# Kernel tuning notes

Measured on AMD Instinct MI355X. Metric: run time of the kernel, lower is better.

Reference implementation:

```python
import jax, jax.numpy as jnp
import numpy as np

N_HEADS = 16
SEG = 64
EPS = 1e-6


def _sigma(x):
    # ELU(x) + 1 kernel feature map (strictly positive)
    return jax.nn.elu(x) + 1.0


def setup_inputs() -> dict:
    key = jax.random.key(0)
    kx, kq, kk, kv, ko = jax.random.split(key, 5)
    B, T, D = 4, 4096, 1024
    scale = D ** -0.5
    return {
        "x": jax.random.normal(kx, (B, T, D), dtype=jnp.float32),
        "W_q": jax.random.normal(kq, (D, D), dtype=jnp.float32) * scale,
        "W_k": jax.random.normal(kk, (D, D), dtype=jnp.float32) * scale,
        "W_v": jax.random.normal(kv, (D, D), dtype=jnp.float32) * scale,
        "W_o": jax.random.normal(ko, (D, D), dtype=jnp.float32) * scale,
        "beta_param": jnp.zeros((N_HEADS,), dtype=jnp.float32),
    }


def _infini_attention(x, W_q, W_k, W_v, W_o, beta_param):
    B, T, D = x.shape
    H = N_HEADS
    dk = D // H
    assert T % SEG == 0
    S = T // SEG

    def proj(W):
        # nn.Linear: x @ W.T ; split heads -> (B,H,T,dk) -> (S,B,H,SEG,dk)
        y = (x @ W.T).reshape(B, T, H, dk).transpose(0, 2, 1, 3)
        return y.reshape(B, H, S, SEG, dk).transpose(2, 0, 1, 3, 4)

    Qs, Ks, Vs = proj(W_q), proj(W_k), proj(W_v)

    beta = jax.nn.sigmoid(beta_param).reshape(1, H, 1, 1)
    causal = jnp.triu(jnp.ones((SEG, SEG), dtype=bool), k=1)
    inv_sqrt_dk = 1.0 / jnp.sqrt(jnp.asarray(dk, x.dtype))

    M0 = jnp.zeros((B, H, dk, dk), dtype=x.dtype)
    z0 = jnp.zeros((B, H, dk), dtype=x.dtype)

    def step(carry, qkv):
        M, z = carry
        q, k, v = qkv  # each (B,H,SEG,dk)
        # Eq.4 memory retrieval
        sq = _sigma(q)
        denom_q = jnp.sum(sq * z[:, :, None, :], axis=-1, keepdims=True) + EPS
        A_mem = jnp.matmul(sq, M) / denom_q
        # local causal softmax attention
        scores = jnp.matmul(q, jnp.swapaxes(k, -2, -1)) * inv_sqrt_dk
        scores = jnp.where(causal, -jnp.inf, scores)
        A_dot = jnp.matmul(jax.nn.softmax(scores, axis=-1), v)
        A_s = beta * A_mem + (1.0 - beta) * A_dot
        # Eq.5 delta-rule memory update
        sk = _sigma(k)
        denom_k = jnp.sum(sk * z[:, :, None, :], axis=-1, keepdims=True) + EPS
        V_prev = jnp.matmul(sk, M) / denom_k
        M_new = M + jnp.einsum("bhtk,bhtv->bhkv", sk, v - V_prev)
        z_new = z + jnp.sum(sk, axis=-2)
        return (M_new, z_new), A_s

    (M, z), outs = jax.lax.scan(step, (M0, z0), (Qs, Ks, Vs))
    # outs: (S,B,H,SEG,dk) -> (B,T,D)
    out = outs.transpose(1, 3, 0, 2, 4).reshape(B, S * SEG, H, dk)
    # careful: need segment-major time ordering -> (B, H, T, dk) then (B,T,H,dk)
    out = outs.transpose(1, 2, 0, 3, 4).reshape(B, H, T, dk)
    out = out.transpose(0, 2, 1, 3).reshape(B, T, D)
    out = out @ W_o.T
    return out, M.mean(0), z.mean(0)


def reference(x, W_q, W_k, W_v, W_o, beta_param):
    return _infini_attention(x, W_q, W_k, W_v, W_o, beta_param)
```

## Files before the change

### kernel.cpp

```cpp
#include <hip/hip_runtime.h>

typedef __bf16 bf16_t;
typedef __bf16 bf16x8 __attribute__((ext_vector_type(8)));
typedef __bf16 bf16x4 __attribute__((ext_vector_type(4)));
typedef float  f32x4  __attribute__((ext_vector_type(4)));

__device__ __forceinline__ void gload16(const bf16_t* g, bf16_t* l) {
    __builtin_amdgcn_global_load_lds(
        (const __attribute__((address_space(1))) void*)(g),
        (__attribute__((address_space(3))) void*)(l), 16, 0, 0);
}

__global__ __launch_bounds__(256) void cast_bf16_kernel(const float* __restrict__ in,
                                                        bf16_t* __restrict__ out, int n4) {
    int i = blockIdx.x * 256 + threadIdx.x;
    if (i >= n4) return;
    f32x4 v = *reinterpret_cast<const f32x4*>(in + (size_t)i * 4);
    bf16x4 o;
    o[0] = (bf16_t)v[0]; o[1] = (bf16_t)v[1]; o[2] = (bf16_t)v[2]; o[3] = (bf16_t)v[3];
    *reinterpret_cast<bf16x4*>(out + (size_t)i * 4) = o;
}

__global__ __launch_bounds__(256) void cast4_kernel(const float* __restrict__ w0,
                                                    const float* __restrict__ w1,
                                                    const float* __restrict__ w2,
                                                    const float* __restrict__ w3,
                                                    bf16_t* __restrict__ o0,
                                                    bf16_t* __restrict__ o1,
                                                    bf16_t* __restrict__ o2,
                                                    bf16_t* __restrict__ o3) {
    int which = blockIdx.x >> 10;
    int i = (blockIdx.x & 1023) * 256 + threadIdx.x;
    const float* in = (which == 0) ? w0 : (which == 1) ? w1 : (which == 2) ? w2 : w3;
    bf16_t*     out = (which == 0) ? o0 : (which == 1) ? o1 : (which == 2) ? o2 : o3;
    f32x4 v = *reinterpret_cast<const f32x4*>(in + (size_t)i * 4);
    bf16x4 o;
    o[0] = (bf16_t)v[0]; o[1] = (bf16_t)v[1]; o[2] = (bf16_t)v[2]; o[3] = (bf16_t)v[3];
    *reinterpret_cast<bf16x4*>(out + (size_t)i * 4) = o;
}

__device__ __forceinline__ bf16x8 sigma8(bf16x8 x) {
    bf16x8 o;
#pragma unroll
    for (int j = 0; j < 8; j++) {
        float f = (float)x[j];
        float sg = f > 0.f ? f + 1.f : __expf(f);
        o[j] = (bf16_t)sg;
    }
    return o;
}

template <int OUT_BF16>
__global__ __launch_bounds__(512, 2) void gemm256(const bf16_t* __restrict__ A,
                                                  const bf16_t* __restrict__ Bm,
                                                  void* __restrict__ Cv,
                                                  int M, int N, int K) {
    __shared__ bf16_t As[4][256 * 32];
    __shared__ bf16_t Bs[4][256 * 32];

    int bid = blockIdx.x;
    int xq = bid & 7, jq = bid >> 3;
    int bm = xq * 8 + (jq >> 2), bn = jq & 3;

    int tid = threadIdx.x;
    int w = tid >> 6, lane = tid & 63;
    int wm = w >> 2, wn = w & 3;
    int lr = lane & 15, lk = lane >> 4;

    int srow = lane >> 2;
    int schunk = (lane & 3) ^ ((lane >> 3) & 3);
    const bf16_t* gA0 = A  + (size_t)(bm * 256 + w * 32 + srow) * K + schunk * 8;
    const bf16_t* gA1 = gA0 + (size_t)16 * K;
    const bf16_t* gB0 = Bm + (size_t)(bn * 256 + w * 32 + srow) * K + schunk * 8;
    const bf16_t* gB1 = gB0 + (size_t)16 * K;
    int lO0 = (w * 32) * 32 + lane * 8;
    int lO1 = (w * 32 + 16) * 32 + lane * 8;

    int chunkb = (lk ^ ((lr >> 1) & 3)) << 4;
    int aoff[8], boff[4];
#pragma unroll
    for (int mi = 0; mi < 8; mi++) aoff[mi] = (wm * 128 + mi * 16 + lr) * 64 + chunkb;
#pragma unroll
    for (int ni = 0; ni < 4; ni++) boff[ni] = (wn * 64 + ni * 16 + lr) * 64 + chunkb;

    f32x4 acc[8][4];
#pragma unroll
    for (int mi = 0; mi < 8; mi++)
#pragma unroll
        for (int ni = 0; ni < 4; ni++) acc[mi][ni] = (f32x4){0.f, 0.f, 0.f, 0.f};

    const int NT = K >> 5;

    auto STAGE = [&](int t) {
        int slot = t & 3;
        size_t ko = (size_t)t * 32;
        gload16(gA0 + ko, &As[slot][lO0]);
        gload16(gA1 + ko, &As[slot][lO1]);
        gload16(gB0 + ko, &Bs[slot][lO0]);
        gload16(gB1 + ko, &Bs[slot][lO1]);
    };

    STAGE(0); STAGE(1); STAGE(2);

#pragma unroll 1
    for (int t = 0; t < NT; ++t) {
        int ahead = NT - 1 - t;
        if (ahead >= 2)      asm volatile("s_waitcnt vmcnt(8)" ::: "memory");
        else if (ahead == 1) asm volatile("s_waitcnt vmcnt(4)" ::: "memory");
        else                 asm volatile("s_waitcnt vmcnt(0)" ::: "memory");
        __builtin_amdgcn_sched_barrier(0);
        __builtin_amdgcn_s_barrier();
        __builtin_amdgcn_sched_barrier(0);

        const char* pa = (const char*)(&As[t & 3][0]);
        const char* pb = (const char*)(&Bs[t & 3][0]);
        bf16x8 af[8], bfr[4];
#pragma unroll
        for (int mi = 0; mi < 8; mi++)
            af[mi] = *reinterpret_cast<const bf16x8*>(pa + aoff[mi]);
#pragma unroll
        for (int ni = 0; ni < 4; ni++)
            bfr[ni] = *reinterpret_cast<const bf16x8*>(pb + boff[ni]);

        if (t + 3 < NT) STAGE(t + 3);

        asm volatile("s_waitcnt lgkmcnt(0)" ::: "memory");
        __builtin_amdgcn_sched_barrier(0);
        __builtin_amdgcn_s_setprio(1);
#pragma unroll
        for (int mi = 0; mi < 8; mi++)
#pragma unroll
            for (int ni = 0; ni < 4; ni++)
                acc[mi][ni] = __builtin_amdgcn_mfma_f32_16x16x32_bf16(af[mi], bfr[ni], acc[mi][ni], 0, 0, 0);
        __builtin_amdgcn_s_setprio(0);
    }

    int row0 = bm * 256 + wm * 128 + lk * 4;
    int col0 = bn * 256 + wn * 64 + lr;
#pragma unroll
    for (int mi = 0; mi < 8; mi++)
#pragma unroll
        for (int ni = 0; ni < 4; ni++)
#pragma unroll
            for (int jj = 0; jj < 4; jj++) {
                size_t idx = (size_t)(row0 + mi * 16 + jj) * N + (col0 + ni * 16);
                float v = acc[mi][ni][jj];
                if (OUT_BF16) reinterpret_cast<bf16_t*>(Cv)[idx] = (bf16_t)v;
                else          reinterpret_cast<float*>(Cv)[idx]  = v;
            }
}

__global__ __launch_bounds__(256) void attn_kernel(const bf16_t* __restrict__ Qb,
                                                   bf16_t* __restrict__ Kb,
                                                   bf16_t* __restrict__ Vb,
                                                   bf16_t* __restrict__ skTg,
                                                   float* __restrict__ csum,
                                                   bf16_t* __restrict__ Adot) {
    __shared__ bf16_t kS[64 * 72];
    __shared__ bf16_t vS[64 * 72];
    __shared__ bf16_t skT[64 * 72];
    __shared__ bf16_t vT[64 * 72];
    __shared__ bf16_t pS[64 * 72];
    __shared__ float  scr[64 * 68];

    int u = blockIdx.x;
    int bh = u >> 6, s = u & 63;
    int b = bh >> 4, h = bh & 15;
    int tid = threadIdx.x;
    int w = tid >> 6, lane = tid & 63;
    int lr = lane & 15, lk = lane >> 4;
    int r = tid >> 2, qd = tid & 3, c0 = qd << 4;

    size_t vseg = ((size_t)b * 4096 + s * 64) * 1024 + (size_t)h * 64;
    size_t sb = ((size_t)bh * 64 + s) * 4096;

    {
        bf16x8 k0 = *reinterpret_cast<const bf16x8*>(Kb + vseg + (size_t)r * 1024 + c0);
        bf16x8 k1 = *reinterpret_cast<const bf16x8*>(Kb + vseg + (size_t)r * 1024 + c0 + 8);
        bf16x8 v0 = *reinterpret_cast<const bf16x8*>(Vb + vseg + (size_t)r * 1024 + c0);
        bf16x8 v1 = *reinterpret_cast<const bf16x8*>(Vb + vseg + (size_t)r * 1024 + c0 + 8);
        *reinterpret_cast<bf16x8*>(&kS[r * 72 + c0])     = k0;
        *reinterpret_cast<bf16x8*>(&kS[r * 72 + c0 + 8]) = k1;
        *reinterpret_cast<bf16x8*>(&vS[r * 72 + c0])     = v0;
        *reinterpret_cast<bf16x8*>(&vS[r * 72 + c0 + 8]) = v1;
        bf16x8 s0 = sigma8(k0), s1 = sigma8(k1);
        *reinterpret_cast<bf16x8*>(Kb + vseg + (size_t)r * 1024 + c0)     = s0;
        *reinterpret_cast<bf16x8*>(Kb + vseg + (size_t)r * 1024 + c0 + 8) = s1;
#pragma unroll
        for (int j = 0; j < 8; j++) {
            skT[(c0 + j) * 72 + r]     = s0[j];
            skT[(c0 + 8 + j) * 72 + r] = s1[j];
            vT[(c0 + j) * 72 + r]      = v0[j];
            vT[(c0 + 8 + j) * 72 + r]  = v1[j];
        }
    }
    __syncthreads();

    if (tid < 64) {
        float acc = 0.f;
#pragma unroll 8
        for (int t = 0; t < 64; t++) acc += (float)skT[tid * 72 + t];
        csum[((size_t)bh * 64 + s) * 64 + tid] = acc;
    }
    *reinterpret_cast<bf16x8*>(skTg + sb + (size_t)r * 64 + c0) =
        *reinterpret_cast<const bf16x8*>(&skT[r * 72 + c0]);
    *reinterpret_cast<bf16x8*>(skTg + sb + (size_t)r * 64 + c0 + 8) =
        *reinterpret_cast<const bf16x8*>(&skT[r * 72 + c0 + 8]);
    *reinterpret_cast<bf16x8*>(Vb + vseg + (size_t)r * 1024 + c0) =
        *reinterpret_cast<const bf16x8*>(&vT[r * 72 + c0]);
    *reinterpret_cast<bf16x8*>(Vb + vseg + (size_t)r * 1024 + c0 + 8) =
        *reinterpret_cast<const bf16x8*>(&vT[r * 72 + c0 + 8]);

    {
        bf16x8 aq[2];
#pragma unroll
        for (int ks = 0; ks < 2; ks++)
            aq[ks] = *reinterpret_cast<const bf16x8*>(Qb + vseg + (size_t)(w * 16 + lr) * 1024 + lk * 8 + ks * 32);
        f32x4 sc[4];
#pragma unroll
        for (int ct = 0; ct < 4; ct++) {
            sc[ct] = (f32x4){0.f, 0.f, 0.f, 0.f};
#pragma unroll
            for (int ks = 0; ks < 2; ks++) {
                bf16x8 bfrag = *reinterpret_cast<const bf16x8*>(&kS[(ct * 16 + lr) * 72 + lk * 8 + ks * 32]);
                sc[ct] = __builtin_amdgcn_mfma_f32_16x16x32_bf16(aq[ks], bfrag, sc[ct], 0, 0, 0);
            }
        }
#pragma unroll
        for (int ct = 0; ct < 4; ct++)
#pragma unroll
            for (int j = 0; j < 4; j++)
                scr[(w * 16 + lk * 4 + j) * 68 + ct * 16 + lr] = sc[ct][j] * 0.125f;
    }
    __syncthreads();

    {
        float p[16];
        float mx = -3.4e38f;
        const float* srow_p = &scr[r * 68 + c0];
#pragma unroll
        for (int i = 0; i < 16; i++) {
            int c = c0 + i;
            float v = (c <= r) ? srow_p[i] : -3.4e38f;
            p[i] = v;
            mx = fmaxf(mx, v);
        }
        mx = fmaxf(mx, __shfl_xor(mx, 1));
        mx = fmaxf(mx, __shfl_xor(mx, 2));
        float sum = 0.f;
#pragma unroll
        for (int i = 0; i < 16; i++) {
            int c = c0 + i;
            float e = (c <= r) ? __expf(p[i] - mx) : 0.f;
            p[i] = e;
            sum += e;
        }
        sum += __shfl_xor(sum, 1);
        sum += __shfl_xor(sum, 2);
        float inv = 1.f / sum;
        bf16x8 p0, p1;
#pragma unroll
        for (int j = 0; j < 8; j++) {
            p0[j] = (bf16_t)(p[j] * inv);
            p1[j] = (bf16_t)(p[8 + j] * inv);
        }
        *reinterpret_cast<bf16x8*>(&pS[r * 72 + c0])     = p0;
        *reinterpret_cast<bf16x8*>(&pS[r * 72 + c0 + 8]) = p1;
    }
    __syncthreads();

    {
        f32x4 ad[4];
#pragma unroll
        for (int ct = 0; ct < 4; ct++) {
            ad[ct] = (f32x4){0.f, 0.f, 0.f, 0.f};
#pragma unroll
            for (int ks = 0; ks < 2; ks++) {
                bf16x8 afrag = *reinterpret_cast<const bf16x8*>(&pS[(w * 16 + lr) * 72 + lk * 8 + ks * 32]);
                bf16x8 bfrag = *reinterpret_cast<const bf16x8*>(&vT[(ct * 16 + lr) * 72 + lk * 8 + ks * 32]);
                ad[ct] = __builtin_amdgcn_mfma_f32_16x16x32_bf16(afrag, bfrag, ad[ct], 0, 0, 0);
            }
        }
#pragma unroll
        for (int ct = 0; ct < 4; ct++)
#pragma unroll
            for (int j = 0; j < 4; j++)
                kS[(w * 16 + lk * 4 + j) * 72 + ct * 16 + lr] = (bf16_t)ad[ct][j];
    }
    __syncthreads();
    *reinterpret_cast<bf16x8*>(Adot + sb + (size_t)r * 64 + c0) =
        *reinterpret_cast<const bf16x8*>(&kS[r * 72 + c0]);
    *reinterpret_cast<bf16x8*>(Adot + sb + (size_t)r * 64 + c0 + 8) =
        *reinterpret_cast<const bf16x8*>(&kS[r * 72 + c0 + 8]);
}

__global__ __launch_bounds__(64) void zprefix_kernel(const float* __restrict__ csum,
                                                     float* __restrict__ zx,
                                                     float* __restrict__ zfin) {
    int bh = blockIdx.x;
    int d = threadIdx.x;
    float c[64];
#pragma unroll
    for (int s = 0; s < 64; s++)
        c[s] = csum[((size_t)bh * 64 + s) * 64 + d];
    float z = 0.f;
#pragma unroll
    for (int s = 0; s < 64; s++) {
        zx[((size_t)bh * 64 + s) * 64 + d] = z;
        z += c[s];
    }
    zfin[bh * 64 + d] = z;
}

__global__ __launch_bounds__(128) void denom_kernel(const bf16_t* __restrict__ Qb,
                                                    const bf16_t* __restrict__ sK,
                                                    const float* __restrict__ zx,
                                                    float* __restrict__ invq,
                                                    float* __restrict__ invk) {
    __shared__ float zL[64];
    int u = blockIdx.x;
    int bh = u >> 6, s = u & 63;
    int b = bh >> 4, h = bh & 15;
    int tid = threadIdx.x;
    if (tid < 64) zL[tid] = zx[((size_t)bh * 64 + s) * 64 + tid];
    __syncthreads();
    int row = tid & 63;
    bool isq = tid < 64;
    const bf16_t* src = (isq ? Qb : sK) +
                        ((size_t)b * 4096 + s * 64 + row) * 1024 + (size_t)h * 64;
    float acc = 0.f;
#pragma unroll
    for (int blk = 0; blk < 8; blk++) {
        bf16x8 v = *reinterpret_cast<const bf16x8*>(src + blk * 8);
#pragma unroll
        for (int j = 0; j < 8; j++) {
            float f = (float)v[j];
            float sg;
            if (isq) {
                sg = f > 0.f ? f + 1.f : __expf(f);
                sg = (float)(bf16_t)sg;
            } else {
                sg = f;
            }
            acc = __builtin_fmaf(sg, zL[blk * 8 + j], acc);
        }
    }
    float inv = 1.f / (acc + 1e-6f);
    float* dst = isq ? invq : invk;
    dst[((size_t)bh * 64 + s) * 64 + row] = inv;
}

__global__ __launch_bounds__(64, 1) void scan_kernel(const bf16_t* __restrict__ sK,
                                                     const bf16_t* __restrict__ vTg,
                                                     const bf16_t* __restrict__ skTg,
                                                     const float* __restrict__ invk,
                                                     bf16_t* __restrict__ Msnap,
                                                     float* __restrict__ Mfin) {
    __shared__ bf16_t MbL[16 * 72];
    __shared__ bf16_t uTL[16 * 72];
    __shared__ float  ikL[64];

    int blk = blockIdx.x;
    int bh = blk & 63, cq = blk >> 6;
    int c0 = cq << 4;
    int b = bh >> 4, h = bh & 15;
    int lane = threadIdx.x;
    int lr = lane & 15, lk = lane >> 4;
    int vr = lane >> 2, vt0 = (lane & 3) << 4;

    size_t chbase = ((size_t)b * 4096) * 1024 + (size_t)h * 64;
    size_t stbase = (size_t)bh * 64 * 4096;

    auto swz = [](bf16_t* base, int row, int intra) -> bf16_t* {
        return (bf16_t*)((char*)base + row * 144 + (intra ^ ((row & 7) << 4)));
    };

    for (int i = lane; i < 16 * 72; i += 64) MbL[i] = (bf16_t)0.f;
    f32x4 Mreg[4];
#pragma unroll
    for (int rt = 0; rt < 4; rt++) Mreg[rt] = (f32x4){0.f, 0.f, 0.f, 0.f};

    bf16x8 cK[4][2], cT[4][2];
#pragma unroll
    for (int rt = 0; rt < 4; rt++)
#pragma unroll
        for (int ks = 0; ks < 2; ks++) {
            cK[rt][ks] = *reinterpret_cast<const bf16x8*>(
                sK + chbase + (size_t)(rt * 16 + lr) * 1024 + lk * 8 + ks * 32);
            cT[rt][ks] = *reinterpret_cast<const bf16x8*>(
                skTg + stbase + (size_t)(rt * 16 + lr) * 64 + lk * 8 + ks * 32);
        }
    {
        bf16x8 v0 = *reinterpret_cast<const bf16x8*>(vTg + chbase + (size_t)(c0 + vr) * 1024 + vt0);
        bf16x8 v1 = *reinterpret_cast<const bf16x8*>(vTg + chbase + (size_t)(c0 + vr) * 1024 + vt0 + 8);
        *reinterpret_cast<bf16x8*>(swz(uTL, vr, vt0 * 2))      = v0;
        *reinterpret_cast<bf16x8*>(swz(uTL, vr, vt0 * 2 + 16)) = v1;
        ikL[lane] = invk[(size_t)bh * 4096 + lane];
    }

    for (int s = 0; s < 64; s++) {
        bf16x8 nK[4][2], nT[4][2], nv0, nv1;
        float nik = 0.f;
        if (s < 63) {
            size_t vs2 = chbase + (size_t)(s + 1) * 65536;
            size_t sb2 = stbase + (size_t)(s + 1) * 4096;
#pragma unroll
            for (int rt = 0; rt < 4; rt++)
#pragma unroll
                for (int ks = 0; ks < 2; ks++) {
                    nK[rt][ks] = *reinterpret_cast<const bf16x8*>(
                        sK + vs2 + (size_t)(rt * 16 + lr) * 1024 + lk * 8 + ks * 32);
                    nT[rt][ks] = *reinterpret_cast<const bf16x8*>(
                        skTg + sb2 + (size_t)(rt * 16 + lr) * 64 + lk * 8 + ks * 32);
                }
            nv0 = *reinterpret_cast<const bf16x8*>(vTg + vs2 + (size_t)(c0 + vr) * 1024 + vt0);
            nv1 = *reinterpret_cast<const bf16x8*>(vTg + vs2 + (size_t)(c0 + vr) * 1024 + vt0 + 8);
            nik = invk[(size_t)bh * 4096 + (size_t)(s + 1) * 64 + lane];
        }

        bf16x8 mb0 = *reinterpret_cast<const bf16x8*>(swz(MbL, lr, lk * 16));
        bf16x8 mb1 = *reinterpret_cast<const bf16x8*>(swz(MbL, lr, lk * 16 + 64));
        f32x4 Y[4];
#pragma unroll
        for (int rt = 0; rt < 4; rt++) {
            Y[rt] = (f32x4){0.f, 0.f, 0.f, 0.f};
            Y[rt] = __builtin_amdgcn_mfma_f32_16x16x32_bf16(cK[rt][0], mb0, Y[rt], 0, 0, 0);
            Y[rt] = __builtin_amdgcn_mfma_f32_16x16x32_bf16(cK[rt][1], mb1, Y[rt], 0, 0, 0);
        }

#pragma unroll
        for (int rt = 0; rt < 4; rt++) {
            bf16x4 vv = *reinterpret_cast<const bf16x4*>(swz(uTL, lr, rt * 32 + lk * 8));
            bf16x4 uu;
#pragma unroll
            for (int j = 0; j < 4; j++) {
                float ik = ikL[rt * 16 + lk * 4 + j];
                uu[j] = (bf16_t)((float)vv[j] - Y[rt][j] * ik);
            }
            *reinterpret_cast<bf16x4*>(swz(uTL, lr, rt * 32 + lk * 8)) = uu;
        }

        bf16x8 ub0 = *reinterpret_cast<const bf16x8*>(swz(uTL, lr, lk * 16));
        bf16x8 ub1 = *reinterpret_cast<const bf16x8*>(swz(uTL, lr, lk * 16 + 64));
#pragma unroll
        for (int rt = 0; rt < 4; rt++) {
            Mreg[rt] = __builtin_amdgcn_mfma_f32_16x16x32_bf16(cT[rt][0], ub0, Mreg[rt], 0, 0, 0);
            Mreg[rt] = __builtin_amdgcn_mfma_f32_16x16x32_bf16(cT[rt][1], ub1, Mreg[rt], 0, 0, 0);
        }

#pragma unroll
        for (int rt = 0; rt < 4; rt++) {
            bf16x4 mp;
#pragma unroll
            for (int j = 0; j < 4; j++) mp[j] = (bf16_t)Mreg[rt][j];
            *reinterpret_cast<bf16x4*>(swz(MbL, lr, rt * 32 + lk * 8)) = mp;
            if (s < 63)
                *reinterpret_cast<bf16x4*>(
                    Msnap + (((size_t)bh * 64 + s + 1) * 64 + c0 + lr) * 64 + rt * 16 + lk * 4) = mp;
        }

        if (s < 63) {
#pragma unroll
            for (int rt = 0; rt < 4; rt++)
#pragma unroll
                for (int ks = 0; ks < 2; ks++) { cK[rt][ks] = nK[rt][ks]; cT[rt][ks] = nT[rt][ks]; }
            *reinterpret_cast<bf16x8*>(swz(uTL, vr, vt0 * 2))      = nv0;
            *reinterpret_cast<bf16x8*>(swz(uTL, vr, vt0 * 2 + 16)) = nv1;
            ikL[lane] = nik;
        }
    }

#pragma unroll
    for (int rt = 0; rt < 4; rt++)
#pragma unroll
        for (int j = 0; j < 4; j++)
            Mfin[(size_t)bh * 4096 + (size_t)(rt * 16 + lk * 4 + j) * 64 + c0 + lr] = Mreg[rt][j];
}

__global__ __launch_bounds__(256) void combine_kernel(const bf16_t* __restrict__ Qb,
                                                      const bf16_t* __restrict__ Msnap,
                                                      const bf16_t* __restrict__ Adot,
                                                      const float* __restrict__ invq,
                                                      const float* __restrict__ beta_param,
                                                      bf16_t* __restrict__ Op) {
    __shared__ bf16_t oS[64 * 72];
    __shared__ bf16_t adS[64 * 72];
    __shared__ float  iq[64];

    int u = blockIdx.x;
    int bh = u >> 6, s = u & 63;
    int b = bh >> 4, h = bh & 15;
    int tid = threadIdx.x;
    int w = tid >> 6, lane = tid & 63;
    int lr = lane & 15, lk = lane >> 4;
    int r = tid >> 2, c0 = (tid & 3) << 4;

    size_t vseg = ((size_t)b * 4096 + s * 64) * 1024 + (size_t)h * 64;
    size_t sb = ((size_t)bh * 64 + s) * 4096;
    size_t ib = ((size_t)bh * 64 + s) * 64;

    float beta = 1.f / (1.f + __expf(-beta_param[h]));
    float omb = 1.f - beta;

    *reinterpret_cast<bf16x8*>(&adS[r * 72 + c0]) =
        *reinterpret_cast<const bf16x8*>(Adot + sb + (size_t)r * 64 + c0);
    *reinterpret_cast<bf16x8*>(&adS[r * 72 + c0 + 8]) =
        *reinterpret_cast<const bf16x8*>(Adot + sb + (size_t)r * 64 + c0 + 8);
    if (tid < 64) iq[tid] = invq[ib + tid];

    f32x4 Y[4];
#pragma unroll
    for (int ct = 0; ct < 4; ct++) Y[ct] = (f32x4){0.f, 0.f, 0.f, 0.f};
    if (s > 0) {
        bf16x8 aq[2];
#pragma unroll
        for (int ks = 0; ks < 2; ks++)
            aq[ks] = sigma8(*reinterpret_cast<const bf16x8*>(
                Qb + vseg + (size_t)(w * 16 + lr) * 1024 + lk * 8 + ks * 32));
#pragma unroll
        for (int ct = 0; ct < 4; ct++)
#pragma unroll
            for (int ks = 0; ks < 2; ks++) {
                bf16x8 bfrag = *reinterpret_cast<const bf16x8*>(
                    Msnap + sb + (size_t)(ct * 16 + lr) * 64 + lk * 8 + ks * 32);
                Y[ct] = __builtin_amdgcn_mfma_f32_16x16x32_bf16(aq[ks], bfrag, Y[ct], 0, 0, 0);
            }
    }
    __syncthreads();

#pragma unroll
    for (int ct = 0; ct < 4; ct++) {
        int colc = ct * 16 + lr;
#pragma unroll
        for (int j = 0; j < 4; j++) {
            int t = w * 16 + lk * 4 + j;
            float o = beta * (Y[ct][j] * iq[t]) + omb * (float)adS[t * 72 + colc];
            oS[t * 72 + colc] = (bf16_t)o;
        }
    }
    __syncthreads();

    *reinterpret_cast<bf16x8*>(Op + vseg + (size_t)r * 1024 + c0) =
        *reinterpret_cast<const bf16x8*>(&oS[r * 72 + c0]);
    *reinterpret_cast<bf16x8*>(Op + vseg + (size_t)r * 1024 + c0 + 8) =
        *reinterpret_cast<const bf16x8*>(&oS[r * 72 + c0 + 8]);
}

__global__ __launch_bounds__(256) void mean_kernel(const float* __restrict__ Mfin,
                                                   const float* __restrict__ zfin,
                                                   float* __restrict__ out) {
    int idx = blockIdx.x * 256 + threadIdx.x;
    if (idx < 65536) {
        out[16777216 + idx] = 0.25f * (Mfin[idx] + Mfin[idx + 65536] +
                                       Mfin[idx + 131072] + Mfin[idx + 196608]);
    } else if (idx < 66560) {
        int j = idx - 65536;
        out[16842752 + j] = 0.25f * (zfin[j] + zfin[j + 1024] + zfin[j + 2048] + zfin[j + 3072]);
    }
}

extern "C" void kernel_launch(void* const* d_in, const int* in_sizes, int n_in,
                              void* d_out, int out_size, void* d_ws, size_t ws_size,
                              hipStream_t stream) {
    const float* x      = (const float*)d_in[0];
    const float* Wq     = (const float*)d_in[1];
    const float* Wk     = (const float*)d_in[2];
    const float* Wv     = (const float*)d_in[3];
    const float* Wo     = (const float*)d_in[4];
    const float* beta_p = (const float*)d_in[5];
    float* out = (float*)d_out;
    char* ws = (char*)d_ws;

    const size_t NX = 16777216ull;

    bf16_t* xb   = (bf16_t*)ws;
    bf16_t* Adot = xb;
    bf16_t* Wqb  = (bf16_t*)(ws + 33554432);
    bf16_t* Wkb  = (bf16_t*)(ws + 35651584);
    bf16_t* Wvb  = (bf16_t*)(ws + 37748736);
    bf16_t* Wob  = (bf16_t*)(ws + 39845888);
    bf16_t* Qb   = (bf16_t*)(ws + 41943040);
    bf16_t* Kb   = (bf16_t*)(ws + 75497472);
    bf16_t* Vb   = (bf16_t*)(ws + 109051904);
    bf16_t* skT  = (bf16_t*)(ws + 142606336);
    bf16_t* Op   = (bf16_t*)(ws + 176160768);
    float*  csum = (float*)(ws + 209715200);
    float*  zx   = (float*)(ws + 210763776);
    float*  invq = (float*)(ws + 211812352);
    float*  invk = (float*)(ws + 212860928);
    float*  Mfin = (float*)(ws + 213909504);
    float*  zfin = (float*)(ws + 214958080);
    bf16_t* Msnap = (bf16_t*)d_out;

    cast_bf16_kernel<<<dim3(16384), dim3(256), 0, stream>>>(x, xb, (int)(NX / 4));
    cast4_kernel<<<dim3(4096), dim3(256), 0, stream>>>(Wq, Wk, Wv, Wo, Wqb, Wkb, Wvb, Wob);

    gemm256<1><<<dim3(256), dim3(512), 0, stream>>>(xb, Wqb, (void*)Qb, 16384, 1024, 1024);
    gemm256<1><<<dim3(256), dim3(512), 0, stream>>>(xb, Wkb, (void*)Kb, 16384, 1024, 1024);
    gemm256<1><<<dim3(256), dim3(512), 0, stream>>>(xb, Wvb, (void*)Vb, 16384, 1024, 1024);

    attn_kernel<<<dim3(4096), dim3(256), 0, stream>>>(Qb, Kb, Vb, skT, csum, Adot);
    zprefix_kernel<<<dim3(64), dim3(64), 0, stream>>>(csum, zx, zfin);
    denom_kernel<<<dim3(4096), dim3(128), 0, stream>>>(Qb, Kb, zx, invq, invk);
    scan_kernel<<<dim3(256), dim3(64), 0, stream>>>(Kb, Vb, skT, invk, Msnap, Mfin);
    combine_kernel<<<dim3(4096), dim3(256), 0, stream>>>(Qb, Msnap, Adot, invq, beta_p, Op);

    gemm256<0><<<dim3(256), dim3(512), 0, stream>>>(Op, Wob, d_out, 16384, 1024, 1024);
    mean_kernel<<<dim3(260), dim3(256), 0, stream>>>(Mfin, zfin, out);
}
```

Baseline: 335.9 us.

## Merge four column-chunk scan blocks into one wave per batch-head

The memory scan kernel now runs one 64-thread block per batch-head and handles all four 16-column chunks of M itself, instead of launching four blocks per batch-head. The aim is to load the sigma(K) and sigma(K)^T fragments once rather than four times, and to let four independent MFMA chains interleave within one wave to hide latency. The cost is fewer waves on the GPU (64 instead of 256) and a four-times longer serial instruction stream per wave, plus higher register pressure from the 4x4 accumulator array.

```diff
diff --git a/kernel.cpp b/kernel.cpp
--- a/kernel.cpp
+++ b/kernel.cpp
@@ -356,13 +356,11 @@
                                                      const float* __restrict__ invk,
                                                      bf16_t* __restrict__ Msnap,
                                                      float* __restrict__ Mfin) {
-    __shared__ bf16_t MbL[16 * 72];
-    __shared__ bf16_t uTL[16 * 72];
+    __shared__ bf16_t MbL[4][16 * 72];
+    __shared__ bf16_t uTL[4][16 * 72];
     __shared__ float  ikL[64];
 
-    int blk = blockIdx.x;
-    int bh = blk & 63, cq = blk >> 6;
-    int c0 = cq << 4;
+    int bh = blockIdx.x;
     int b = bh >> 4, h = bh & 15;
     int lane = threadIdx.x;
     int lr = lane & 15, lk = lane >> 4;
@@ -375,10 +373,15 @@
         return (bf16_t*)((char*)base + row * 144 + (intra ^ ((row & 7) << 4)));
     };
 
-    for (int i = lane; i < 16 * 72; i += 64) MbL[i] = (bf16_t)0.f;
-    f32x4 Mreg[4];
-#pragma unroll
-    for (int rt = 0; rt < 4; rt++) Mreg[rt] = (f32x4){0.f, 0.f, 0.f, 0.f};
+    for (int i = lane; i < 16 * 72; i += 64) {
+        MbL[0][i] = (bf16_t)0.f; MbL[1][i] = (bf16_t)0.f;
+        MbL[2][i] = (bf16_t)0.f; MbL[3][i] = (bf16_t)0.f;
+    }
+    f32x4 Mreg[4][4];
+#pragma unroll
+    for (int c = 0; c < 4; c++)
+#pragma unroll
+        for (int rt = 0; rt < 4; rt++) Mreg[c][rt] = (f32x4){0.f, 0.f, 0.f, 0.f};
 
     bf16x8 cK[4][2], cT[4][2];
 #pragma unroll
@@ -390,16 +393,18 @@
             cT[rt][ks] = *reinterpret_cast<const bf16x8*>(
                 skTg + stbase + (size_t)(rt * 16 + lr) * 64 + lk * 8 + ks * 32);
         }
-    {
-        bf16x8 v0 = *reinterpret_cast<const bf16x8*>(vTg + chbase + (size_t)(c0 + vr) * 1024 + vt0);
-        bf16x8 v1 = *reinterpret_cast<const bf16x8*>(vTg + chbase + (size_t)(c0 + vr) * 1024 + vt0 + 8);
-        *reinterpret_cast<bf16x8*>(swz(uTL, vr, vt0 * 2))      = v0;
-        *reinterpret_cast<bf16x8*>(swz(uTL, vr, vt0 * 2 + 16)) = v1;
-        ikL[lane] = invk[(size_t)bh * 4096 + lane];
-    }
-
+#pragma unroll
+    for (int c = 0; c < 4; c++) {
+        bf16x8 v0 = *reinterpret_cast<const bf16x8*>(vTg + chbase + (size_t)(c * 16 + vr) * 1024 + vt0);
+        bf16x8 v1 = *reinterpret_cast<const bf16x8*>(vTg + chbase + (size_t)(c * 16 + vr) * 1024 + vt0 + 8);
+        *reinterpret_cast<bf16x8*>(swz(&uTL[c][0], vr, vt0 * 2))      = v0;
+        *reinterpret_cast<bf16x8*>(swz(&uTL[c][0], vr, vt0 * 2 + 16)) = v1;
+    }
+    ikL[lane] = invk[(size_t)bh * 4096 + lane];
+
+#pragma unroll 1
     for (int s = 0; s < 64; s++) {
-        bf16x8 nK[4][2], nT[4][2], nv0, nv1;
+        bf16x8 nK[4][2], nT[4][2], nv[4][2];
         float nik = 0.f;
         if (s < 63) {
             size_t vs2 = chbase + (size_t)(s + 1) * 65536;
@@ -413,50 +418,67 @@
                     nT[rt][ks] = *reinterpret_cast<const bf16x8*>(
                         skTg + sb2 + (size_t)(rt * 16 + lr) * 64 + lk * 8 + ks * 32);
                 }
-            nv0 = *reinterpret_cast<const bf16x8*>(vTg + vs2 + (size_t)(c0 + vr) * 1024 + vt0);
-            nv1 = *reinterpret_cast<const bf16x8*>(vTg + vs2 + (size_t)(c0 + vr) * 1024 + vt0 + 8);
+#pragma unroll
+            for (int c = 0; c < 4; c++) {
+                nv[c][0] = *reinterpret_cast<const bf16x8*>(vTg + vs2 + (size_t)(c * 16 + vr) * 1024 + vt0);
+                nv[c][1] = *reinterpret_cast<const bf16x8*>(vTg + vs2 + (size_t)(c * 16 + vr) * 1024 + vt0 + 8);
+            }
             nik = invk[(size_t)bh * 4096 + (size_t)(s + 1) * 64 + lane];
         }
 
-        bf16x8 mb0 = *reinterpret_cast<const bf16x8*>(swz(MbL, lr, lk * 16));
-        bf16x8 mb1 = *reinterpret_cast<const bf16x8*>(swz(MbL, lr, lk * 16 + 64));
-        f32x4 Y[4];
-#pragma unroll
-        for (int rt = 0; rt < 4; rt++) {
-            Y[rt] = (f32x4){0.f, 0.f, 0.f, 0.f};
-            Y[rt] = __builtin_amdgcn_mfma_f32_16x16x32_bf16(cK[rt][0], mb0, Y[rt], 0, 0, 0);
-            Y[rt] = __builtin_amdgcn_mfma_f32_16x16x32_bf16(cK[rt][1], mb1, Y[rt], 0, 0, 0);
-        }
-
-#pragma unroll
-        for (int rt = 0; rt < 4; rt++) {
-            bf16x4 vv = *reinterpret_cast<const bf16x4*>(swz(uTL, lr, rt * 32 + lk * 8));
-            bf16x4 uu;
-#pragma unroll
-            for (int j = 0; j < 4; j++) {
-                float ik = ikL[rt * 16 + lk * 4 + j];
-                uu[j] = (bf16_t)((float)vv[j] - Y[rt][j] * ik);
-            }
-            *reinterpret_cast<bf16x4*>(swz(uTL, lr, rt * 32 + lk * 8)) = uu;
-        }
-
-        bf16x8 ub0 = *reinterpret_cast<const bf16x8*>(swz(uTL, lr, lk * 16));
-        bf16x8 ub1 = *reinterpret_cast<const bf16x8*>(swz(uTL, lr, lk * 16 + 64));
-#pragma unroll
-        for (int rt = 0; rt < 4; rt++) {
-            Mreg[rt] = __builtin_amdgcn_mfma_f32_16x16x32_bf16(cT[rt][0], ub0, Mreg[rt], 0, 0, 0);
-            Mreg[rt] = __builtin_amdgcn_mfma_f32_16x16x32_bf16(cT[rt][1], ub1, Mreg[rt], 0, 0, 0);
-        }
-
-#pragma unroll
-        for (int rt = 0; rt < 4; rt++) {
-            bf16x4 mp;
-#pragma unroll
-            for (int j = 0; j < 4; j++) mp[j] = (bf16_t)Mreg[rt][j];
-            *reinterpret_cast<bf16x4*>(swz(MbL, lr, rt * 32 + lk * 8)) = mp;
-            if (s < 63)
-                *reinterpret_cast<bf16x4*>(
-                    Msnap + (((size_t)bh * 64 + s + 1) * 64 + c0 + lr) * 64 + rt * 16 + lk * 4) = mp;
+        bf16x8 mb0[4], mb1[4];
+#pragma unroll
+        for (int c = 0; c < 4; c++) {
+            mb0[c] = *reinterpret_cast<const bf16x8*>(swz(&MbL[c][0], lr, lk * 16));
+            mb1[c] = *reinterpret_cast<const bf16x8*>(swz(&MbL[c][0], lr, lk * 16 + 64));
+        }
+
+#pragma unroll
+        for (int c = 0; c < 4; c++) {
+            f32x4 Y[4];
+#pragma unroll
+            for (int rt = 0; rt < 4; rt++) {
+                Y[rt] = (f32x4){0.f, 0.f, 0.f, 0.f};
+                Y[rt] = __builtin_amdgcn_mfma_f32_16x16x32_bf16(cK[rt][0], mb0[c], Y[rt], 0, 0, 0);
+                Y[rt] = __builtin_amdgcn_mfma_f32_16x16x32_bf16(cK[rt][1], mb1[c], Y[rt], 0, 0, 0);
+            }
+#pragma unroll
+            for (int rt = 0; rt < 4; rt++) {
+                bf16x4 vv = *reinterpret_cast<const bf16x4*>(swz(&uTL[c][0], lr, rt * 32 + lk * 8));
+                bf16x4 uu;
+#pragma unroll
+                for (int j = 0; j < 4; j++) {
+                    float ik = ikL[rt * 16 + lk * 4 + j];
+                    uu[j] = (bf16_t)((float)vv[j] - Y[rt][j] * ik);
+                }
+                *reinterpret_cast<bf16x4*>(swz(&uTL[c][0], lr, rt * 32 + lk * 8)) = uu;
+            }
+        }
+
+        bf16x8 ub0[4], ub1[4];
+#pragma unroll
+        for (int c = 0; c < 4; c++) {
+            ub0[c] = *reinterpret_cast<const bf16x8*>(swz(&uTL[c][0], lr, lk * 16));
+            ub1[c] = *reinterpret_cast<const bf16x8*>(swz(&uTL[c][0], lr, lk * 16 + 64));
+        }
+
+#pragma unroll
+        for (int c = 0; c < 4; c++) {
+#pragma unroll
+            for (int rt = 0; rt < 4; rt++) {
+                Mreg[c][rt] = __builtin_amdgcn_mfma_f32_16x16x32_bf16(cT[rt][0], ub0[c], Mreg[c][rt], 0, 0, 0);
+                Mreg[c][rt] = __builtin_amdgcn_mfma_f32_16x16x32_bf16(cT[rt][1], ub1[c], Mreg[c][rt], 0, 0, 0);
+            }
+#pragma unroll
+            for (int rt = 0; rt < 4; rt++) {
+                bf16x4 mp;
+#pragma unroll
+                for (int j = 0; j < 4; j++) mp[j] = (bf16_t)Mreg[c][rt][j];
+                *reinterpret_cast<bf16x4*>(swz(&MbL[c][0], lr, rt * 32 + lk * 8)) = mp;
+                if (s < 63)
+                    *reinterpret_cast<bf16x4*>(
+                        Msnap + (((size_t)bh * 64 + s + 1) * 64 + c * 16 + lr) * 64 + rt * 16 + lk * 4) = mp;
+            }
         }
 
         if (s < 63) {
@@ -464,17 +486,22 @@
             for (int rt = 0; rt < 4; rt++)
 #pragma unroll
                 for (int ks = 0; ks < 2; ks++) { cK[rt][ks] = nK[rt][ks]; cT[rt][ks] = nT[rt][ks]; }
-            *reinterpret_cast<bf16x8*>(swz(uTL, vr, vt0 * 2))      = nv0;
-            *reinterpret_cast<bf16x8*>(swz(uTL, vr, vt0 * 2 + 16)) = nv1;
+#pragma unroll
+            for (int c = 0; c < 4; c++) {
+                *reinterpret_cast<bf16x8*>(swz(&uTL[c][0], vr, vt0 * 2))      = nv[c][0];
+                *reinterpret_cast<bf16x8*>(swz(&uTL[c][0], vr, vt0 * 2 + 16)) = nv[c][1];
+            }
             ikL[lane] = nik;
         }
     }
 
 #pragma unroll
-    for (int rt = 0; rt < 4; rt++)
-#pragma unroll
-        for (int j = 0; j < 4; j++)
-            Mfin[(size_t)bh * 4096 + (size_t)(rt * 16 + lk * 4 + j) * 64 + c0 + lr] = Mreg[rt][j];
+    for (int c = 0; c < 4; c++)
+#pragma unroll
+        for (int rt = 0; rt < 4; rt++)
+#pragma unroll
+            for (int j = 0; j < 4; j++)
+                Mfin[(size_t)bh * 4096 + (size_t)(rt * 16 + lk * 4 + j) * 64 + c * 16 + lr] = Mreg[c][rt][j];
 }
 
 __global__ __launch_bounds__(256) void combine_kernel(const bf16_t* __restrict__ Qb,
@@ -602,7 +629,7 @@
     attn_kernel<<<dim3(4096), dim3(256), 0, stream>>>(Qb, Kb, Vb, skT, csum, Adot);
     zprefix_kernel<<<dim3(64), dim3(64), 0, stream>>>(csum, zx, zfin);
     denom_kernel<<<dim3(4096), dim3(128), 0, stream>>>(Qb, Kb, zx, invq, invk);
-    scan_kernel<<<dim3(256), dim3(64), 0, stream>>>(Kb, Vb, skT, invk, Msnap, Mfin);
+    scan_kernel<<<dim3(64), dim3(64), 0, stream>>>(Kb, Vb, skT, invk, Msnap, Mfin);
     combine_kernel<<<dim3(4096), dim3(256), 0, stream>>>(Qb, Msnap, Adot, invq, beta_p, Op);
 
     gemm256<0><<<dim3(256), dim3(512), 0, stream>>>(Op, Wob, d_out, 16384, 1024, 1024);
```

New measurement: 401.4 us. +19.5%, slower.

## Fuse Q, K, V projections into one GEMM with interleaved QKV layout

Applied to the files above, without the earlier changes.

Replaces three separate x@W GEMM launches with a single GEMM of N=3072 writing an interleaved QKV buffer of row stride 3072, relying on Wq/Wk/Wv bf16 copies being contiguous in workspace. All downstream kernels (attention, denom, scan, combine) are re-addressed to read Q, K and V from the strided buffer. The GEMM tile mapping is generalised to arbitrary N with an XCD-aware remap. This is meant to cut launch overhead and fill the GPU better with 768 workgroups, at the cost of more strided memory access downstream.

```diff
diff --git a/kernel.cpp b/kernel.cpp
--- a/kernel.cpp
+++ b/kernel.cpp
@@ -4,6 +4,8 @@
 typedef __bf16 bf16x8 __attribute__((ext_vector_type(8)));
 typedef __bf16 bf16x4 __attribute__((ext_vector_type(4)));
 typedef float  f32x4  __attribute__((ext_vector_type(4)));
+
+#define QKV_STR 3072
 
 __device__ __forceinline__ void gload16(const bf16_t* g, bf16_t* l) {
     __builtin_amdgcn_global_load_lds(
@@ -58,9 +60,11 @@
     __shared__ bf16_t As[4][256 * 32];
     __shared__ bf16_t Bs[4][256 * 32];
 
+    int nbn = N >> 8;
+    int nwg = (M >> 8) * nbn;
     int bid = blockIdx.x;
-    int xq = bid & 7, jq = bid >> 3;
-    int bm = xq * 8 + (jq >> 2), bn = jq & 3;
+    int wg = ((nwg & 7) == 0) ? ((bid & 7) * (nwg >> 3) + (bid >> 3)) : bid;
+    int bm = wg / nbn, bn = wg % nbn;
 
     int tid = threadIdx.x;
     int w = tid >> 6, lane = tid & 63;
@@ -150,9 +154,7 @@
             }
 }
 
-__global__ __launch_bounds__(256) void attn_kernel(const bf16_t* __restrict__ Qb,
-                                                   bf16_t* __restrict__ Kb,
-                                                   bf16_t* __restrict__ Vb,
+__global__ __launch_bounds__(256) void attn_kernel(bf16_t* __restrict__ QKV,
                                                    bf16_t* __restrict__ skTg,
                                                    float* __restrict__ csum,
                                                    bf16_t* __restrict__ Adot) {
@@ -171,21 +173,23 @@
     int lr = lane & 15, lk = lane >> 4;
     int r = tid >> 2, qd = tid & 3, c0 = qd << 4;
 
-    size_t vseg = ((size_t)b * 4096 + s * 64) * 1024 + (size_t)h * 64;
+    bf16_t* qp = QKV + (size_t)(b * 4096 + s * 64) * QKV_STR + (size_t)h * 64;
+    bf16_t* kp = qp + 1024;
+    bf16_t* vp = qp + 2048;
     size_t sb = ((size_t)bh * 64 + s) * 4096;
 
     {
-        bf16x8 k0 = *reinterpret_cast<const bf16x8*>(Kb + vseg + (size_t)r * 1024 + c0);
-        bf16x8 k1 = *reinterpret_cast<const bf16x8*>(Kb + vseg + (size_t)r * 1024 + c0 + 8);
-        bf16x8 v0 = *reinterpret_cast<const bf16x8*>(Vb + vseg + (size_t)r * 1024 + c0);
-        bf16x8 v1 = *reinterpret_cast<const bf16x8*>(Vb + vseg + (size_t)r * 1024 + c0 + 8);
+        bf16x8 k0 = *reinterpret_cast<const bf16x8*>(kp + (size_t)r * QKV_STR + c0);
+        bf16x8 k1 = *reinterpret_cast<const bf16x8*>(kp + (size_t)r * QKV_STR + c0 + 8);
+        bf16x8 v0 = *reinterpret_cast<const bf16x8*>(vp + (size_t)r * QKV_STR + c0);
+        bf16x8 v1 = *reinterpret_cast<const bf16x8*>(vp + (size_t)r * QKV_STR + c0 + 8);
         *reinterpret_cast<bf16x8*>(&kS[r * 72 + c0])     = k0;
         *reinterpret_cast<bf16x8*>(&kS[r * 72 + c0 + 8]) = k1;
         *reinterpret_cast<bf16x8*>(&vS[r * 72 + c0])     = v0;
         *reinterpret_cast<bf16x8*>(&vS[r * 72 + c0 + 8]) = v1;
         bf16x8 s0 = sigma8(k0), s1 = sigma8(k1);
-        *reinterpret_cast<bf16x8*>(Kb + vseg + (size_t)r * 1024 + c0)     = s0;
-        *reinterpret_cast<bf16x8*>(Kb + vseg + (size_t)r * 1024 + c0 + 8) = s1;
+        *reinterpret_cast<bf16x8*>(kp + (size_t)r * QKV_STR + c0)     = s0;
+        *reinterpret_cast<bf16x8*>(kp + (size_t)r * QKV_STR + c0 + 8) = s1;
 #pragma unroll
         for (int j = 0; j < 8; j++) {
             skT[(c0 + j) * 72 + r]     = s0[j];
@@ -206,16 +210,16 @@
         *reinterpret_cast<const bf16x8*>(&skT[r * 72 + c0]);
     *reinterpret_cast<bf16x8*>(skTg + sb + (size_t)r * 64 + c0 + 8) =
         *reinterpret_cast<const bf16x8*>(&skT[r * 72 + c0 + 8]);
-    *reinterpret_cast<bf16x8*>(Vb + vseg + (size_t)r * 1024 + c0) =
+    *reinterpret_cast<bf16x8*>(vp + (size_t)r * QKV_STR + c0) =
         *reinterpret_cast<const bf16x8*>(&vT[r * 72 + c0]);
-    *reinterpret_cast<bf16x8*>(Vb + vseg + (size_t)r * 1024 + c0 + 8) =
+    *reinterpret_cast<bf16x8*>(vp + (size_t)r * QKV_STR + c0 + 8) =
         *reinterpret_cast<const bf16x8*>(&vT[r * 72 + c0 + 8]);
 
     {
         bf16x8 aq[2];
 #pragma unroll
         for (int ks = 0; ks < 2; ks++)
-            aq[ks] = *reinterpret_cast<const bf16x8*>(Qb + vseg + (size_t)(w * 16 + lr) * 1024 + lk * 8 + ks * 32);
+            aq[ks] = *reinterpret_cast<const bf16x8*>(qp + (size_t)(w * 16 + lr) * QKV_STR + lk * 8 + ks * 32);
         f32x4 sc[4];
 #pragma unroll
         for (int ct = 0; ct < 4; ct++) {
@@ -312,8 +316,7 @@
     zfin[bh * 64 + d] = z;
 }
 
-__global__ __launch_bounds__(128) void denom_kernel(const bf16_t* __restrict__ Qb,
-                                                    const bf16_t* __restrict__ sK,
+__global__ __launch_bounds__(128) void denom_kernel(const bf16_t* __restrict__ QKV,
                                                     const float* __restrict__ zx,
                                                     float* __restrict__ invq,
                                                     float* __restrict__ invk) {
@@ -326,8 +329,8 @@
     __syncthreads();
     int row = tid & 63;
     bool isq = tid < 64;
-    const bf16_t* src = (isq ? Qb : sK) +
-                        ((size_t)b * 4096 + s * 64 + row) * 1024 + (size_t)h * 64;
+    const bf16_t* src = QKV + (size_t)(b * 4096 + s * 64 + row) * QKV_STR +
+                        (size_t)h * 64 + (isq ? 0 : 1024);
     float acc = 0.f;
 #pragma unroll
     for (int blk = 0; blk < 8; blk++) {
@@ -350,8 +353,7 @@
     dst[((size_t)bh * 64 + s) * 64 + row] = inv;
 }
 
-__global__ __launch_bounds__(64, 1) void scan_kernel(const bf16_t* __restrict__ sK,
-                                                     const bf16_t* __restrict__ vTg,
+__global__ __launch_bounds__(64, 1) void scan_kernel(const bf16_t* __restrict__ QKV,
                                                      const bf16_t* __restrict__ skTg,
                                                      const float* __restrict__ invk,
                                                      bf16_t* __restrict__ Msnap,
@@ -368,8 +370,11 @@
     int lr = lane & 15, lk = lane >> 4;
     int vr = lane >> 2, vt0 = (lane & 3) << 4;
 
-    size_t chbase = ((size_t)b * 4096) * 1024 + (size_t)h * 64;
+    const bf16_t* sKb = QKV + 1024;
+    const bf16_t* vTb = QKV + 2048;
+    size_t chbase = (size_t)(b * 4096) * QKV_STR + (size_t)h * 64;
     size_t stbase = (size_t)bh * 64 * 4096;
+    const size_t SEG = (size_t)64 * QKV_STR;
 
     auto swz = [](bf16_t* base, int row, int intra) -> bf16_t* {
         return (bf16_t*)((char*)base + row * 144 + (intra ^ ((row & 7) << 4)));
@@ -386,13 +391,13 @@
 #pragma unroll
         for (int ks = 0; ks < 2; ks++) {
             cK[rt][ks] = *reinterpret_cast<const bf16x8*>(
-                sK + chbase + (size_t)(rt * 16 + lr) * 1024 + lk * 8 + ks * 32);
+                sKb + chbase + (size_t)(rt * 16 + lr) * QKV_STR + lk * 8 + ks * 32);
             cT[rt][ks] = *reinterpret_cast<const bf16x8*>(
                 skTg + stbase + (size_t)(rt * 16 + lr) * 64 + lk * 8 + ks * 32);
         }
     {
-        bf16x8 v0 = *reinterpret_cast<const bf16x8*>(vTg + chbase + (size_t)(c0 + vr) * 1024 + vt0);
-        bf16x8 v1 = *reinterpret_cast<const bf16x8*>(vTg + chbase + (size_t)(c0 + vr) * 1024 + vt0 + 8);
+        bf16x8 v0 = *reinterpret_cast<const bf16x8*>(vTb + chbase + (size_t)(c0 + vr) * QKV_STR + vt0);
+        bf16x8 v1 = *reinterpret_cast<const bf16x8*>(vTb + chbase + (size_t)(c0 + vr) * QKV_STR + vt0 + 8);
         *reinterpret_cast<bf16x8*>(swz(uTL, vr, vt0 * 2))      = v0;
         *reinterpret_cast<bf16x8*>(swz(uTL, vr, vt0 * 2 + 16)) = v1;
         ikL[lane] = invk[(size_t)bh * 4096 + lane];
@@ -402,19 +407,19 @@
         bf16x8 nK[4][2], nT[4][2], nv0, nv1;
         float nik = 0.f;
         if (s < 63) {
-            size_t vs2 = chbase + (size_t)(s + 1) * 65536;
+            size_t vs2 = chbase + (size_t)(s + 1) * SEG;
             size_t sb2 = stbase + (size_t)(s + 1) * 4096;
 #pragma unroll
             for (int rt = 0; rt < 4; rt++)
 #pragma unroll
                 for (int ks = 0; ks < 2; ks++) {
                     nK[rt][ks] = *reinterpret_cast<const bf16x8*>(
-                        sK + vs2 + (size_t)(rt * 16 + lr) * 1024 + lk * 8 + ks * 32);
+                        sKb + vs2 + (size_t)(rt * 16 + lr) * QKV_STR + lk * 8 + ks * 32);
                     nT[rt][ks] = *reinterpret_cast<const bf16x8*>(
                         skTg + sb2 + (size_t)(rt * 16 + lr) * 64 + lk * 8 + ks * 32);
                 }
-            nv0 = *reinterpret_cast<const bf16x8*>(vTg + vs2 + (size_t)(c0 + vr) * 1024 + vt0);
-            nv1 = *reinterpret_cast<const bf16x8*>(vTg + vs2 + (size_t)(c0 + vr) * 1024 + vt0 + 8);
+            nv0 = *reinterpret_cast<const bf16x8*>(vTb + vs2 + (size_t)(c0 + vr) * QKV_STR + vt0);
+            nv1 = *reinterpret_cast<const bf16x8*>(vTb + vs2 + (size_t)(c0 + vr) * QKV_STR + vt0 + 8);
             nik = invk[(size_t)bh * 4096 + (size_t)(s + 1) * 64 + lane];
         }
 
@@ -477,7 +482,7 @@
             Mfin[(size_t)bh * 4096 + (size_t)(rt * 16 + lk * 4 + j) * 64 + c0 + lr] = Mreg[rt][j];
 }
 
-__global__ __launch_bounds__(256) void combine_kernel(const bf16_t* __restrict__ Qb,
+__global__ __launch_bounds__(256) void combine_kernel(const bf16_t* __restrict__ QKV,
                                                       const bf16_t* __restrict__ Msnap,
                                                       const bf16_t* __restrict__ Adot,
                                                       const float* __restrict__ invq,
@@ -495,7 +500,8 @@
     int lr = lane & 15, lk = lane >> 4;
     int r = tid >> 2, c0 = (tid & 3) << 4;
 
-    size_t vseg = ((size_t)b * 4096 + s * 64) * 1024 + (size_t)h * 64;
+    const bf16_t* qp = QKV + (size_t)(b * 4096 + s * 64) * QKV_STR + (size_t)h * 64;
+    size_t vsegO = ((size_t)b * 4096 + s * 64) * 1024 + (size_t)h * 64;
     size_t sb = ((size_t)bh * 64 + s) * 4096;
     size_t ib = ((size_t)bh * 64 + s) * 64;
 
@@ -516,7 +522,7 @@
 #pragma unroll
         for (int ks = 0; ks < 2; ks++)
             aq[ks] = sigma8(*reinterpret_cast<const bf16x8*>(
-                Qb + vseg + (size_t)(w * 16 + lr) * 1024 + lk * 8 + ks * 32));
+                qp + (size_t)(w * 16 + lr) * QKV_STR + lk * 8 + ks * 32));
 #pragma unroll
         for (int ct = 0; ct < 4; ct++)
 #pragma unroll
@@ -540,9 +546,9 @@
     }
     __syncthreads();
 
-    *reinterpret_cast<bf16x8*>(Op + vseg + (size_t)r * 1024 + c0) =
+    *reinterpret_cast<bf16x8*>(Op + vsegO + (size_t)r * 1024 + c0) =
         *reinterpret_cast<const bf16x8*>(&oS[r * 72 + c0]);
-    *reinterpret_cast<bf16x8*>(Op + vseg + (size_t)r * 1024 + c0 + 8) =
+    *reinterpret_cast<bf16x8*>(Op + vsegO + (size_t)r * 1024 + c0 + 8) =
         *reinterpret_cast<const bf16x8*>(&oS[r * 72 + c0 + 8]);
 }
 
@@ -579,9 +585,7 @@
     bf16_t* Wkb  = (bf16_t*)(ws + 35651584);
     bf16_t* Wvb  = (bf16_t*)(ws + 37748736);
     bf16_t* Wob  = (bf16_t*)(ws + 39845888);
-    bf16_t* Qb   = (bf16_t*)(ws + 41943040);
-    bf16_t* Kb   = (bf16_t*)(ws + 75497472);
-    bf16_t* Vb   = (bf16_t*)(ws + 109051904);
+    bf16_t* QKV  = (bf16_t*)(ws + 41943040);
     bf16_t* skT  = (bf16_t*)(ws + 142606336);
     bf16_t* Op   = (bf16_t*)(ws + 176160768);
     float*  csum = (float*)(ws + 209715200);
@@ -595,15 +599,13 @@
     cast_bf16_kernel<<<dim3(16384), dim3(256), 0, stream>>>(x, xb, (int)(NX / 4));
     cast4_kernel<<<dim3(4096), dim3(256), 0, stream>>>(Wq, Wk, Wv, Wo, Wqb, Wkb, Wvb, Wob);
 
-    gemm256<1><<<dim3(256), dim3(512), 0, stream>>>(xb, Wqb, (void*)Qb, 16384, 1024, 1024);
-    gemm256<1><<<dim3(256), dim3(512), 0, stream>>>(xb, Wkb, (void*)Kb, 16384, 1024, 1024);
-    gemm256<1><<<dim3(256), dim3(512), 0, stream>>>(xb, Wvb, (void*)Vb, 16384, 1024, 1024);
-
-    attn_kernel<<<dim3(4096), dim3(256), 0, stream>>>(Qb, Kb, Vb, skT, csum, Adot);
+    gemm256<1><<<dim3(768), dim3(512), 0, stream>>>(xb, Wqb, (void*)QKV, 16384, 3072, 1024);
+
+    attn_kernel<<<dim3(4096), dim3(256), 0, stream>>>(QKV, skT, csum, Adot);
     zprefix_kernel<<<dim3(64), dim3(64), 0, stream>>>(csum, zx, zfin);
-    denom_kernel<<<dim3(4096), dim3(128), 0, stream>>>(Qb, Kb, zx, invq, invk);
-    scan_kernel<<<dim3(256), dim3(64), 0, stream>>>(Kb, Vb, skT, invk, Msnap, Mfin);
-    combine_kernel<<<dim3(4096), dim3(256), 0, stream>>>(Qb, Msnap, Adot, invq, beta_p, Op);
+    denom_kernel<<<dim3(4096), dim3(128), 0, stream>>>(QKV, zx, invq, invk);
+    scan_kernel<<<dim3(256), dim3(64), 0, stream>>>(QKV, skT, invk, Msnap, Mfin);
+    combine_kernel<<<dim3(4096), dim3(256), 0, stream>>>(QKV, Msnap, Adot, invq, beta_p, Op);
 
     gemm256<0><<<dim3(256), dim3(512), 0, stream>>>(Op, Wob, d_out, 16384, 1024, 1024);
     mean_kernel<<<dim3(260), dim3(256), 0, stream>>>(Mfin, zfin, out);
```

After: 337.9 us. About the same (+0.6%).
